# Kernel tuning notes

Measured on AMD Instinct MI355X. Metric: run time of the kernel, lower is better.

The kernel has to match this reference:

```python
import jax, jax.numpy as jnp
import numpy as np

N_BLOCKS = 12   # grid rows == cols
D = 256         # per-block feature size (small -> memory-bound)
BATCH = 8192    # samples per block

# Deterministic block-sparse pattern: block (i, j) is active iff (i - j) % 3 == 0.
_mask = np.array([[(i - j) % 3 == 0 for j in range(N_BLOCKS)] for i in range(N_BLOCKS)])
_I, _J = np.nonzero(_mask)  # 48 active blocks
N_ACTIVE = _I.shape[0]


def setup_inputs() -> dict:
    key = jax.random.key(0)
    k1, k2, k3 = jax.random.split(key, 3)
    X = jax.random.normal(k1, (N_BLOCKS, BATCH, D), dtype=jnp.float32)
    # One Linear(D, D) per active block: weight [K, D_in, D_out], bias [K, D_out]
    W = jax.random.normal(k2, (N_ACTIVE, D, D), dtype=jnp.float32) / np.sqrt(D).astype(np.float32)
    b = jax.random.normal(k3, (N_ACTIVE, D), dtype=jnp.float32) * 0.01
    i_idx = jnp.asarray(_I, dtype=jnp.int32)  # output-row index of each active block
    j_idx = jnpim if False else jnp.asarray(_J, dtype=jnp.int32)  # input-col index of each active block
    return {"X": X, "W": W, "b": b, "i_idx": i_idx, "j_idx": j_idx}


def reference(X, W, b, i_idx, j_idx):
    # Gather the input block feeding each active sub-module: [K, BATCH, D]
    Xg = X[j_idx]
    # Apply each block's Linear in one batched contraction: [K, BATCH, D]
    h = jnp.einsum('kbi,kio->kbo', Xg, W) + b[:, None, :]
    # Sum block outputs into their output rows (the '+' combiner / safe_sum):
    # rows with no active block get an all-zero output, matching the zero-vector semantics.
    y = jax.ops.segment_sum(h, i_idx, num_segments=N_BLOCKS)  # [N_BLOCKS, BATCH, D]
    return y
```

## Files before the change

kernel.cpp:

```cpp
#include <hip/hip_runtime.h>

#define N_BLOCKS 12
#define D 256
#define BATCH 8192

typedef __attribute__((ext_vector_type(8))) short bf16x8;
typedef __attribute__((ext_vector_type(4))) float f32x4;

__device__ __forceinline__ unsigned short f2bf(float f) {
  unsigned int u = __float_as_uint(f);
  u += 0x7fffu + ((u >> 16) & 1u);
  return (unsigned short)(u >> 16);
}

__device__ __forceinline__ void gld16(const unsigned short* g, unsigned short* l) {
  __builtin_amdgcn_global_load_lds(
      (const __attribute__((address_space(1))) unsigned int*)g,
      (__attribute__((address_space(3))) unsigned int*)l,
      16, 0, 0);
}

__global__ void cvt_x(const float* __restrict__ X, unsigned short* __restrict__ Xb) {
  const long long t = (long long)blockIdx.x * 256 + threadIdx.x;
  const long long base = t * 8;
  const float4 v0 = *(const float4*)(X + base);
  const float4 v1 = *(const float4*)(X + base + 4);
  uint4 r;
  r.x = (unsigned)f2bf(v0.x) | ((unsigned)f2bf(v0.y) << 16);
  r.y = (unsigned)f2bf(v0.z) | ((unsigned)f2bf(v0.w) << 16);
  r.z = (unsigned)f2bf(v1.x) | ((unsigned)f2bf(v1.y) << 16);
  r.w = (unsigned)f2bf(v1.z) | ((unsigned)f2bf(v1.w) << 16);
  *(uint4*)(Xb + base) = r;
}

__global__ void cvt_w(const float* __restrict__ W, unsigned short* __restrict__ Wt) {
  __shared__ unsigned short tile[32][33];
  const int k  = blockIdx.x >> 6;
  const int t  = blockIdx.x & 63;
  const int ti = t >> 3;
  const int tj = t & 7;
  const float* Wk = W + (long long)k * D * D;
  unsigned short* Wtk = Wt + (long long)k * D * D;
  const int lx = threadIdx.x & 31, ly = threadIdx.x >> 5;
  #pragma unroll
  for (int r = 0; r < 4; ++r) {
    const int i = ti * 32 + ly + r * 8;
    const int o = tj * 32 + lx;
    tile[ly + r * 8][lx] = f2bf(Wk[i * D + o]);
  }
  __syncthreads();
  #pragma unroll
  for (int r = 0; r < 4; ++r) {
    const int o = tj * 32 + ly + r * 8;
    const int i = ti * 32 + lx;
    Wtk[o * D + i] = tile[lx][ly + r * 8];
  }
}

__launch_bounds__(512, 4)
__global__ void bs_gemm(const unsigned short* __restrict__ Xb,
                        const unsigned short* __restrict__ Wt,
                        const float* __restrict__ bias,
                        const int* __restrict__ i_idx,
                        const int* __restrict__ j_idx,
                        int nact,
                        float* __restrict__ Y) {
  __shared__ unsigned short lds[3 * 12288];

  const int bid   = blockIdx.x;
  const int xcd   = bid & 7;
  const int local = bid >> 3;
  const int pp    = local >> 5;
  const int bm    = local & 31;
  const int p     = xcd * 3 + pp;
  const int i     = p >> 1;
  const int bn    = p & 1;

  int ks0 = 0, ks1 = 0, ks2 = 0, ks3 = 0, js0 = 0, js1 = 0, js2 = 0, js3 = 0, nk = 0;
  for (int k = 0; k < nact; ++k) {
    if (i_idx[k] == i) {
      const int j = j_idx[k];
      if      (nk == 0) { ks0 = k; js0 = j; }
      else if (nk == 1) { ks1 = k; js1 = j; }
      else if (nk == 2) { ks2 = k; js2 = j; }
      else              { ks3 = k; js3 = j; }
      ++nk;
    }
  }
#define JS(t) ((t) == 0 ? js0 : (t) == 1 ? js1 : (t) == 2 ? js2 : js3)
#define KS(t) ((t) == 0 ? ks0 : (t) == 1 ? ks1 : (t) == 2 ? ks2 : ks3)

  const int tid  = threadIdx.x;
  const int wave = tid >> 6;
  const int lane = tid & 63;
  const int wm   = wave >> 1;
  const int wn   = wave & 1;
  const int q    = lane >> 4;
  const int l15  = lane & 15;

  const int srow = tid >> 2;
  const int sc   = (tid & 3) ^ (srow & 3);
  const long long sA0 = (long long)srow * D + sc * 8;
  const long long sA1 = (long long)(srow + 128) * D + sc * 8;
  const long long sB0 = (long long)srow * D + sc * 8;
  const int dA0 = tid * 8;
  const int dA1 = 4096 + tid * 8;
  const int dB0 = 8192 + tid * 8;

  const int sw  = (q ^ (l15 & 3)) << 4;
  const int aR0 = (wm * 64 +  0 + l15) * 64 + sw;
  const int aR1 = (wm * 64 + 16 + l15) * 64 + sw;
  const int aR2 = (wm * 64 + 32 + l15) * 64 + sw;
  const int aR3 = (wm * 64 + 48 + l15) * 64 + sw;
  const int bR0 = 16384 + (wn * 64 +  0 + l15) * 64 + sw;
  const int bR1 = 16384 + (wn * 64 + 16 + l15) * 64 + sw;
  const int bR2 = 16384 + (wn * 64 + 32 + l15) * 64 + sw;
  const int bR3 = 16384 + (wn * 64 + 48 + l15) * 64 + sw;

  auto STAGE = [&](int st) {
    const int t  = st >> 3;
    const int kk = st & 7;
    unsigned short* sl = lds + (st % 3) * 12288;
    const unsigned short* As =
        Xb + ((long long)JS(t) * BATCH + bm * 256) * D + kk * 32;
    const unsigned short* Bs =
        Wt + ((long long)KS(t) * D + bn * 128) * D + kk * 32;
    gld16(As + sA0, sl + dA0);
    gld16(As + sA1, sl + dA1);
    gld16(Bs + sB0, sl + dB0);
  };

  f32x4 acc[4][4] = {};

  STAGE(0);
  STAGE(1);

  #pragma unroll
  for (int kt = 0; kt < 32; ++kt) {
    if (kt == 31) asm volatile("s_waitcnt vmcnt(0)" ::: "memory");
    else          asm volatile("s_waitcnt vmcnt(3)" ::: "memory");
    __builtin_amdgcn_s_barrier();
    __builtin_amdgcn_sched_barrier(0);

    const char* sb = (const char*)(lds + (kt % 3) * 12288);
    bf16x8 aF[4], bF[4];
    aF[0] = *(const bf16x8*)(sb + aR0);
    aF[1] = *(const bf16x8*)(sb + aR1);
    aF[2] = *(const bf16x8*)(sb + aR2);
    aF[3] = *(const bf16x8*)(sb + aR3);
    bF[0] = *(const bf16x8*)(sb + bR0);
    bF[1] = *(const bf16x8*)(sb + bR1);
    bF[2] = *(const bf16x8*)(sb + bR2);
    bF[3] = *(const bf16x8*)(sb + bR3);

    if (kt < 30) STAGE(kt + 2);

    asm volatile("s_waitcnt lgkmcnt(0)" ::: "memory");
    __builtin_amdgcn_sched_barrier(0);

    __builtin_amdgcn_s_setprio(1);
    #pragma unroll
    for (int mf = 0; mf < 4; ++mf)
      #pragma unroll
      for (int nf = 0; nf < 4; ++nf)
        acc[mf][nf] = __builtin_amdgcn_mfma_f32_16x16x32_bf16(
            aF[mf], bF[nf], acc[mf][nf], 0, 0, 0);
    __builtin_amdgcn_s_setprio(0);
  }

  float* Yb = Y + (long long)i * BATCH * D;
  const int m0 = bm * 256 + wm * 64 + q * 4;
  const int n0 = bn * 128 + wn * 64 + l15;
  float bsum[4];
  #pragma unroll
  for (int nf = 0; nf < 4; ++nf) {
    float s = 0.f;
    for (int t = 0; t < nk; ++t) s += bias[KS(t) * D + n0 + nf * 16];
    bsum[nf] = s;
  }
  #pragma unroll
  for (int nf = 0; nf < 4; ++nf) {
    #pragma unroll
    for (int mf = 0; mf < 4; ++mf)
      #pragma unroll
      for (int r2 = 0; r2 < 4; ++r2)
        Yb[(long long)(m0 + mf * 16 + r2) * D + (n0 + nf * 16)] =
            acc[mf][nf][r2] + bsum[nf];
  }
#undef JS
#undef KS
}

extern "C" void kernel_launch(void* const* d_in, const int* in_sizes, int n_in,
                              void* d_out, int out_size, void* d_ws, size_t ws_size,
                              hipStream_t stream) {
  const float* X = (const float*)d_in[0];
  const float* W = (const float*)d_in[1];
  const float* b = (const float*)d_in[2];
  const int* i_idx = (const int*)d_in[3];
  const int* j_idx = (const int*)d_in[4];
  float* Y = (float*)d_out;
  const int nact = in_sizes[3];

  unsigned short* Xb = (unsigned short*)d_ws;
  unsigned short* Wt = (unsigned short*)((char*)d_ws + (size_t)N_BLOCKS * BATCH * D * 2);

  cvt_x<<<(N_BLOCKS * BATCH * D) / (256 * 8), 256, 0, stream>>>(X, Xb);
  cvt_w<<<nact * 64, 256, 0, stream>>>(W, Wt);
  bs_gemm<<<N_BLOCKS * 32 * 2, 512, 0, stream>>>(Xb, Wt, b, i_idx, j_idx, nact, Y);
}
```

Baseline: 276.7 us.

## Halve GEMM M-tile, deepen LDS prefetch to five stages, remap blocks

The block-sparse GEMM tile shrinks from 256 to 128 rows, which doubles the grid and halves the per-wave accumulator set. The LDS ring grows from 3 to 5 stages, so four k-steps are prefetched ahead with matching vmcnt waits. The block-to-XCD mapping is reorganised, and the XOR swizzle on LDS reads is removed. The aim is better wave balance and deeper latency hiding, at the cost of more B-tile rereads and possible LDS bank conflicts without the swizzle.

```diff
diff --git a/kernel.cpp b/kernel.cpp
--- a/kernel.cpp
+++ b/kernel.cpp
@@ -65,16 +65,15 @@
                         const int* __restrict__ j_idx,
                         int nact,
                         float* __restrict__ Y) {
-  __shared__ unsigned short lds[3 * 12288];
-
-  const int bid   = blockIdx.x;
-  const int xcd   = bid & 7;
-  const int local = bid >> 3;
-  const int pp    = local >> 5;
-  const int bm    = local & 31;
-  const int p     = xcd * 3 + pp;
-  const int i     = p >> 1;
-  const int bn    = p & 1;
+  __shared__ unsigned short lds[5 * 8192];
+
+  const int bid = blockIdx.x;
+  const int x   = bid & 7;
+  const int r   = bid >> 3;
+  const int i   = r >> 4;
+  const int rem = r & 15;
+  const int bm  = x * 8 + (rem >> 1);
+  const int bn  = rem & 1;
 
   int ks0 = 0, ks1 = 0, ks2 = 0, ks3 = 0, js0 = 0, js1 = 0, js2 = 0, js3 = 0, nk = 0;
   for (int k = 0; k < nact; ++k) {
@@ -98,69 +97,60 @@
   const int q    = lane >> 4;
   const int l15  = lane & 15;
 
-  const int srow = tid >> 2;
-  const int sc   = (tid & 3) ^ (srow & 3);
-  const long long sA0 = (long long)srow * D + sc * 8;
-  const long long sA1 = (long long)(srow + 128) * D + sc * 8;
-  const long long sB0 = (long long)srow * D + sc * 8;
-  const int dA0 = tid * 8;
-  const int dA1 = 4096 + tid * 8;
-  const int dB0 = 8192 + tid * 8;
-
-  const int sw  = (q ^ (l15 & 3)) << 4;
-  const int aR0 = (wm * 64 +  0 + l15) * 64 + sw;
-  const int aR1 = (wm * 64 + 16 + l15) * 64 + sw;
-  const int aR2 = (wm * 64 + 32 + l15) * 64 + sw;
-  const int aR3 = (wm * 64 + 48 + l15) * 64 + sw;
-  const int bR0 = 16384 + (wn * 64 +  0 + l15) * 64 + sw;
-  const int bR1 = 16384 + (wn * 64 + 16 + l15) * 64 + sw;
-  const int bR2 = 16384 + (wn * 64 + 32 + l15) * 64 + sw;
-  const int bR3 = 16384 + (wn * 64 + 48 + l15) * 64 + sw;
+  const int g_off = (tid >> 2) * D + (tid & 3) * 8;
+  const int dA = tid * 8;
+  const int dB = 4096 + tid * 8;
+
+  const int aR0 = (wm * 32 +  0 + l15) * 64 + q * 16;
+  const int aR1 = (wm * 32 + 16 + l15) * 64 + q * 16;
+  const int bB  = 8192;
+  const int bR0 = bB + (wn * 64 +  0 + l15) * 64 + q * 16;
+  const int bR1 = bB + (wn * 64 + 16 + l15) * 64 + q * 16;
+  const int bR2 = bB + (wn * 64 + 32 + l15) * 64 + q * 16;
+  const int bR3 = bB + (wn * 64 + 48 + l15) * 64 + q * 16;
 
   auto STAGE = [&](int st) {
     const int t  = st >> 3;
     const int kk = st & 7;
-    unsigned short* sl = lds + (st % 3) * 12288;
+    unsigned short* sl = lds + (st % 5) * 8192;
     const unsigned short* As =
-        Xb + ((long long)JS(t) * BATCH + bm * 256) * D + kk * 32;
+        Xb + ((long long)JS(t) * BATCH + bm * 128) * D + kk * 32 + g_off;
     const unsigned short* Bs =
-        Wt + ((long long)KS(t) * D + bn * 128) * D + kk * 32;
-    gld16(As + sA0, sl + dA0);
-    gld16(As + sA1, sl + dA1);
-    gld16(Bs + sB0, sl + dB0);
+        Wt + ((long long)KS(t) * D + bn * 128) * D + kk * 32 + g_off;
+    gld16(As, sl + dA);
+    gld16(Bs, sl + dB);
   };
 
-  f32x4 acc[4][4] = {};
-
-  STAGE(0);
-  STAGE(1);
+  f32x4 acc[2][4] = {};
+
+  STAGE(0); STAGE(1); STAGE(2); STAGE(3);
 
   #pragma unroll
   for (int kt = 0; kt < 32; ++kt) {
-    if (kt == 31) asm volatile("s_waitcnt vmcnt(0)" ::: "memory");
-    else          asm volatile("s_waitcnt vmcnt(3)" ::: "memory");
+    if      (kt <= 28) asm volatile("s_waitcnt vmcnt(6)" ::: "memory");
+    else if (kt == 29) asm volatile("s_waitcnt vmcnt(4)" ::: "memory");
+    else if (kt == 30) asm volatile("s_waitcnt vmcnt(2)" ::: "memory");
+    else               asm volatile("s_waitcnt vmcnt(0)" ::: "memory");
     __builtin_amdgcn_s_barrier();
     __builtin_amdgcn_sched_barrier(0);
 
-    const char* sb = (const char*)(lds + (kt % 3) * 12288);
-    bf16x8 aF[4], bF[4];
+    const char* sb = (const char*)lds + (kt % 5) * 16384;
+    bf16x8 aF[2], bF[4];
     aF[0] = *(const bf16x8*)(sb + aR0);
     aF[1] = *(const bf16x8*)(sb + aR1);
-    aF[2] = *(const bf16x8*)(sb + aR2);
-    aF[3] = *(const bf16x8*)(sb + aR3);
     bF[0] = *(const bf16x8*)(sb + bR0);
     bF[1] = *(const bf16x8*)(sb + bR1);
     bF[2] = *(const bf16x8*)(sb + bR2);
     bF[3] = *(const bf16x8*)(sb + bR3);
 
-    if (kt < 30) STAGE(kt + 2);
+    if (kt < 28) STAGE(kt + 4);
 
     asm volatile("s_waitcnt lgkmcnt(0)" ::: "memory");
     __builtin_amdgcn_sched_barrier(0);
 
     __builtin_amdgcn_s_setprio(1);
     #pragma unroll
-    for (int mf = 0; mf < 4; ++mf)
+    for (int mf = 0; mf < 2; ++mf)
       #pragma unroll
       for (int nf = 0; nf < 4; ++nf)
         acc[mf][nf] = __builtin_amdgcn_mfma_f32_16x16x32_bf16(
@@ -169,7 +159,7 @@
   }
 
   float* Yb = Y + (long long)i * BATCH * D;
-  const int m0 = bm * 256 + wm * 64 + q * 4;
+  const int m0 = bm * 128 + wm * 32 + q * 4;
   const int n0 = bn * 128 + wn * 64 + l15;
   float bsum[4];
   #pragma unroll
@@ -181,7 +171,7 @@
   #pragma unroll
   for (int nf = 0; nf < 4; ++nf) {
     #pragma unroll
-    for (int mf = 0; mf < 4; ++mf)
+    for (int mf = 0; mf < 2; ++mf)
       #pragma unroll
       for (int r2 = 0; r2 < 4; ++r2)
         Yb[(long long)(m0 + mf * 16 + r2) * D + (n0 + nf * 16)] =
@@ -207,5 +197,5 @@
 
   cvt_x<<<(N_BLOCKS * BATCH * D) / (256 * 8), 256, 0, stream>>>(X, Xb);
   cvt_w<<<nact * 64, 256, 0, stream>>>(W, Wt);
-  bs_gemm<<<N_BLOCKS * 32 * 2, 512, 0, stream>>>(Xb, Wt, b, i_idx, j_idx, nact, Y);
-}
+  bs_gemm<<<N_BLOCKS * 64 * 2, 512, 0, stream>>>(Xb, Wt, b, i_idx, j_idx, nact, Y);
+}
```

Result: faster. 260.1 us (-6.0%).
